# Optimization experiments

Measured on AMD Instinct MI355X. Metric: run time of the kernel, lower is better.

## Reference

```python
import jax, jax.numpy as jnp
import numpy as np

BN_EPS = 1e-3  # keras BatchNormalization default epsilon


def conv1x1(x, w):
    # x: [N,C,H,W], w: [O,C] (1x1 conv, no bias)
    return jnp.einsum('nchw,oc->nohw', x, w)


def bn(x, gamma, beta, mean, var):
    # inference-mode batchnorm over channel axis 1
    scale = gamma / jnp.sqrt(var + BN_EPS)
    shift = beta - mean * scale
    return x * scale[None, :, None, None] + shift[None, :, None, None]


def fourier_unit(x, w, gamma, beta, mean, var):
    # x: [N,C,H,W] NCHW. 1D rfft over W (matches tf.signal.rfft), normalized by sqrt(W).
    N, C, H, W = x.shape
    norm = jnp.sqrt(jnp.float32(W))
    f = jnp.fft.rfft(x / norm, axis=-1)          # [N,C,H,Wf] complex64, Wf=W//2+1
    Wf = f.shape[-1]
    # interleave re/im per channel: [N,C,2,H,Wf] -> [N,2C,H,Wf]
    ff = jnp.stack([jnp.real(f), jnp.imag(f)], axis=2).reshape(N, 2 * C, H, Wf)
    y = jax.nn.relu(bn(conv1x1(ff, w), gamma, beta, mean, var))  # [N,2C,H,Wf]
    Co = y.shape[1] // 2
    y = y.reshape(N, Co, 2, H, Wf)
    c = jax.lax.complex(y[:, :, 0], y[:, :, 1])
    return jnp.fft.irfft(c, n=W, axis=-1) * norm  # [N,Co,H,W]


def setup_inputs() -> dict:
    key = jax.random.key(0)
    ks = jax.random.split(key, 20)
    N, H, W, Cin = 8, 128, 128, 256
    fmaps = 256
    half = fmaps // 2  # 128

    def nrm(k, shape, s=0.05):
        return jax.random.normal(k, shape, dtype=jnp.float32) * s

    def bn_params(k, c):
        k1, k2, k3, k4 = jax.random.split(k, 4)
        gamma = jax.random.uniform(k1, (c,), dtype=jnp.float32) + 0.5
        beta = nrm(k2, (c,), 0.1)
        mean = nrm(k3, (c,), 0.1)
        var = jax.random.uniform(k4, (c,), dtype=jnp.float32) + 0.5
        return gamma, beta, mean, var

    x = jax.random.normal(ks[0], (N, H, W, Cin), dtype=jnp.float32)
    w1 = nrm(ks[1], (half, Cin))
    g1, b1, m1, v1 = bn_params(ks[2], half)
    fu_w = nrm(ks[3], (2 * half, 2 * half))
    fu_g, fu_b, fu_m, fu_v = bn_params(ks[4], 2 * half)
    lfu_w = nrm(ks[5], (2 * half, 2 * half))
    lfu_g, lfu_b, lfu_m, lfu_v = bn_params(ks[6], 2 * half)
    w2 = nrm(ks[7], (fmaps, half))
    return {
        'x': x, 'w1': w1, 'g1': g1, 'b1': b1, 'm1': m1, 'v1': v1,
        'fu_w': fu_w, 'fu_g': fu_g, 'fu_b': fu_b, 'fu_m': fu_m, 'fu_v': fu_v,
        'lfu_w': lfu_w, 'lfu_g': lfu_g, 'lfu_b': lfu_b, 'lfu_m': lfu_m, 'lfu_v': lfu_v,
        'w2': w2,
    }


def reference(x, w1, g1, b1, m1, v1,
              fu_w, fu_g, fu_b, fu_m, fu_v,
              lfu_w, lfu_g, lfu_b, lfu_m, lfu_v,
              w2):
    # NHWC -> NCHW (stride=1, no downsample)
    x = jnp.transpose(x, (0, 3, 1, 2))
    x = jax.nn.relu(bn(conv1x1(x, w1), g1, b1, m1, v1))  # [N,half,H,W]
    out = fourier_unit(x, fu_w, fu_g, fu_b, fu_m, fu_v)
    # local fourier unit: take first C//4 channels, fold 2x2 spatial patches into channels
    C = x.shape[1]
    xs = x[:, :C // 4]
    xs = jnp.concatenate(jnp.split(xs, 2, axis=2), axis=1)  # split H
    xs = jnp.concatenate(jnp.split(xs, 2, axis=3), axis=1)  # split W -> [N,C,H/2,W/2]
    xs = fourier_unit(xs, lfu_w, lfu_g, lfu_b, lfu_m, lfu_v)
    xs = jnp.tile(xs, (1, 1, 2, 2))  # back to [N,C,H,W]
    out = conv1x1(x + out + xs, w2)  # [N,fmaps,H,W]
    return jnp.transpose(out, (0, 2, 3, 1))  # NCHW -> NHWC
```

## Files before the change

kernel.cpp:

```cpp
#include <hip/hip_runtime.h>
#include <math.h>

typedef __attribute__((ext_vector_type(8))) short short8;
typedef __attribute__((ext_vector_type(4))) float f32x4;
typedef __attribute__((ext_vector_type(16))) float f32x16;

#define SW7b(r) (((r) & 7) << 4)
#define SW3b(r) (((r) & 3) << 4)
#define K15(r) (((r) & 15) << 4)
#define K7(r)  (((r) & 7) << 4)

static __device__ __forceinline__ unsigned short f2b(float f){
  unsigned u = __float_as_uint(f);
  u = (u + 0x7FFFu + ((u >> 16) & 1u)) >> 16;
  return (unsigned short)u;
}
static __device__ __forceinline__ float b2f(unsigned short u){
  return __uint_as_float(((unsigned)u) << 16);
}
static __device__ __forceinline__ void gl16(const void* g, void* l) {
  __builtin_amdgcn_global_load_lds(
      (const __attribute__((address_space(1))) void*)g,
      (__attribute__((address_space(3))) void*)l, 16, 0, 0);
}

__global__ void k_wt(const float* __restrict__ w1, const float* __restrict__ fu_w,
                     const float* __restrict__ lfu_w, const float* __restrict__ w2,
                     const float* __restrict__ g1, const float* __restrict__ b1,
                     const float* __restrict__ m1, const float* __restrict__ v1,
                     const float* __restrict__ fg, const float* __restrict__ fb,
                     const float* __restrict__ fm, const float* __restrict__ fv,
                     const float* __restrict__ lg_, const float* __restrict__ lb_,
                     const float* __restrict__ lm_, const float* __restrict__ lv_,
                     unsigned short* __restrict__ w1b, unsigned short* __restrict__ fuwb,
                     unsigned short* __restrict__ lfuwb, unsigned short* __restrict__ w2b,
                     unsigned short* __restrict__ DFTf, unsigned short* __restrict__ IDFTf,
                     unsigned short* __restrict__ DFTl, unsigned short* __restrict__ IDFTl,
                     float* __restrict__ sc1, float* __restrict__ sh1,
                     float* __restrict__ scF, float* __restrict__ shF,
                     float* __restrict__ scL, float* __restrict__ shL) {
  int t = blockIdx.x * 256 + threadIdx.x;
  const float TPI = 6.283185307179586f;
  if (t < 32768) {
    { int co = t >> 8, k = t & 255; w1b[co * 256 + (k ^ ((co & 7) << 3))] = f2b(w1[t]); }
    { int co = t >> 7, k = t & 127; w2b[co * 128 + (k ^ ((co & 15) << 3))] = f2b(w2[t]); }
  }
  if (t < 65536) {
    int co = t >> 8, k = t & 255;
    fuwb[(size_t)(k >> 6) * 16384 + co * 64 + ((k & 63) ^ ((co & 7) << 3))] = f2b(fu_w[t]);
    lfuwb[co * 256 + (k ^ ((co & 7) << 3))] = f2b(lfu_w[t]);
  }
  if (t < 20480) {
    int m = t >> 7, w = t & 127; float v = 0.f;
    if (m < 130) {
      int wf = m >> 1; int ph = (wf * w) & 127;
      float ang = TPI * (float)ph / 128.f;
      v = ((m & 1) ? -sinf(ang) : cosf(ang)) * 0.08838834764831845f;
    }
    DFTf[m * 128 + (w ^ ((m & 15) << 3))] = f2b(v);
  }
  if (t < 24576) {
    int m = t / 192, k2 = t % 192; float v = 0.f;
    if (k2 < 130) {
      int wf = k2 >> 1; float a = (wf == 0 || wf == 64) ? 1.f : 2.f;
      int ph = (wf * m) & 127;
      float ang = TPI * (float)ph / 128.f;
      v = ((k2 & 1) ? -a * sinf(ang) : a * cosf(ang)) * 0.08838834764831845f;
    }
    IDFTf[m * 192 + (k2 ^ ((m & 7) << 3))] = f2b(v);
  }
  if (t < 5120) {
    int m = t >> 6, w = t & 63; float v = 0.f;
    if (m < 66) {
      int wf = m >> 1; int ph = (wf * w) & 63;
      float ang = TPI * (float)ph / 64.f;
      v = ((m & 1) ? -sinf(ang) : cosf(ang)) * 0.125f;
    }
    DFTl[m * 64 + (w ^ ((m & 7) << 3))] = f2b(v);
  }
  if (t < 6144) {
    int m = t / 96, k2 = t % 96; float v = 0.f;
    if (k2 < 66) {
      int wf = k2 >> 1; float a = (wf == 0 || wf == 32) ? 1.f : 2.f;
      int ph = (wf * m) & 63;
      float ang = TPI * (float)ph / 64.f;
      v = ((k2 & 1) ? -a * sinf(ang) : a * cosf(ang)) * 0.125f;
    }
    IDFTl[m * 96 + (k2 ^ ((m & 3) << 3))] = f2b(v);
  }
  if (t < 128) { float s = g1[t] * rsqrtf(v1[t] + 1e-3f); sc1[t] = s; sh1[t] = b1[t] - m1[t] * s; }
  if (t < 256) { float s = fg[t] * rsqrtf(fv[t] + 1e-3f); scF[t] = s; shF[t] = fb[t] - fm[t] * s; }
  if (t < 256) { float s = lg_[t] * rsqrtf(lv_[t] + 1e-3f); scL[t] = s; shL[t] = lb_[t] - lm_[t] * s; }
}

__global__ __launch_bounds__(512) void k_conv1(const unsigned short* __restrict__ A,
                                               const float* __restrict__ x,
                                               unsigned short* __restrict__ X1c,
                                               const float* __restrict__ scp,
                                               const float* __restrict__ shp) {
  __shared__ __align__(16) char A_s[128 * 512];
  __shared__ __align__(16) char B_s[2][32768];
  int t = threadIdx.x; int wid = t >> 6, l = t & 63;
  int wm = wid >> 2, wn = wid & 3;
  int m0 = wm * 64, n0 = wn * 64;
  int lr = l & 15, lg = l >> 4;
  size_t nh0 = (size_t)blockIdx.x * 2;
  const char* Ab = (const char*)A;
  const char* xrow = (const char*)(x + nh0 * 32768);
  #pragma unroll
  for (int i = 0; i < 8; i++) { int g = i * 512 + t; gl16(Ab + g * 16, A_s + g * 16); }
  #pragma unroll
  for (int i = 0; i < 4; i++) {
    int g = i * 512 + t; int w = g >> 3, o = g & 7;
    gl16(xrow + (size_t)w * 1024 + ((o * 16) ^ SW7b(w)), B_s[0] + g * 16);
  }
  f32x4 acc[4][4];
  #pragma unroll
  for (int mt = 0; mt < 4; mt++)
    #pragma unroll
    for (int nt = 0; nt < 4; nt++) acc[mt][nt] = (f32x4){0.f, 0.f, 0.f, 0.f};
  __syncthreads();
  for (int it = 0; it < 8; it++) {
    int kk = it * 32;
    if (it < 7) {
      #pragma unroll
      for (int i = 0; i < 4; i++) {
        int g = i * 512 + t; int w = g >> 3, o = g & 7;
        gl16(xrow + (size_t)w * 1024 + (kk + 32) * 4 + ((o * 16) ^ SW7b(w)),
             B_s[(it + 1) & 1] + g * 16);
      }
    }
    const char* Bc = B_s[it & 1];
    short8 af[4], bf[4];
    #pragma unroll
    for (int mt = 0; mt < 4; mt++) {
      int m = m0 + 16 * mt + lr;
      af[mt] = *(const short8*)(A_s + m * 512 + ((kk * 2 + lg * 16) ^ SW7b(m)));
    }
    #pragma unroll
    for (int nt = 0; nt < 4; nt++) {
      int w = n0 + 16 * nt + lr;
      float4 f0 = *(const float4*)(Bc + w * 128 + ((lg * 32) ^ SW7b(w)));
      float4 f1 = *(const float4*)(Bc + w * 128 + ((lg * 32 + 16) ^ SW7b(w)));
      short8 bb;
      bb[0] = (short)f2b(f0.x); bb[1] = (short)f2b(f0.y);
      bb[2] = (short)f2b(f0.z); bb[3] = (short)f2b(f0.w);
      bb[4] = (short)f2b(f1.x); bb[5] = (short)f2b(f1.y);
      bb[6] = (short)f2b(f1.z); bb[7] = (short)f2b(f1.w);
      bf[nt] = bb;
    }
    #pragma unroll
    for (int mt = 0; mt < 4; mt++)
      #pragma unroll
      for (int nt = 0; nt < 4; nt++)
        acc[mt][nt] = __builtin_amdgcn_mfma_f32_16x16x32_bf16(af[mt], bf[nt], acc[mt][nt], 0, 0, 0);
    __syncthreads();
  }
  #pragma unroll
  for (int nt = 0; nt < 4; nt++) {
    int wcol = n0 + 16 * nt + lr;
    char* xout = (char*)X1c + (nh0 + (wcol >> 7)) * 32768;
    int w = wcol & 127;
    #pragma unroll
    for (int mt = 0; mt < 4; mt++) {
      int rb = m0 + 16 * mt + lg * 4;
      float4 s4 = *(const float4*)&scp[rb];
      float4 h4 = *(const float4*)&shp[rb];
      f32x4 v = acc[mt][nt];
      *(unsigned short*)(xout + (rb + 0) * 256 + ((w * 2) ^ K15(rb + 0))) = f2b(fmaxf(v[0] * s4.x + h4.x, 0.f));
      *(unsigned short*)(xout + (rb + 1) * 256 + ((w * 2) ^ K15(rb + 1))) = f2b(fmaxf(v[1] * s4.y + h4.y, 0.f));
      *(unsigned short*)(xout + (rb + 2) * 256 + ((w * 2) ^ K15(rb + 2))) = f2b(fmaxf(v[2] * s4.z + h4.z, 0.f));
      *(unsigned short*)(xout + (rb + 3) * 256 + ((w * 2) ^ K15(rb + 3))) = f2b(fmaxf(v[3] * s4.w + h4.w, 0.f));
    }
  }
}

__global__ __launch_bounds__(256) void k_lfu(const unsigned short* __restrict__ DFTm,
                                             const unsigned short* __restrict__ lfuw,
                                             const unsigned short* __restrict__ IDFTm,
                                             const unsigned short* __restrict__ X1c,
                                             const float* __restrict__ scp,
                                             const float* __restrict__ shp,
                                             unsigned short* __restrict__ XSO) {
  __shared__ __align__(16) char SH[81920];
  char* M   = SH;
  char* Xs  = SH + 16384;
  char* FFl = SH + 32768;
  char* Yl  = SH + 57344;
  int t = threadIdx.x, wid = t >> 6, l = t & 63, lr = l & 15, lg = l >> 4;
  int b = blockIdx.x; int n = b >> 6, h2 = b & 63;
  {
    const char* src = (const char*)DFTm;
    #pragma unroll
    for (int i = 0; i < 3; i++) { int g = i * 256 + t; if (g < 640) gl16(src + g * 16, M + g * 16); }
    #pragma unroll
    for (int i = 0; i < 4; i++) {
      int g = i * 256 + t; int c2 = g >> 3, o = g & 7;
      int c0 = c2 & 31, hb = (c2 >> 5) & 1, wbq = (c2 >> 6) & 1;
      int half = wbq ^ ((c0 >> 3) & 1);
      const char* s = (const char*)X1c +
          ((size_t)(n * 128 + hb * 64 + h2) * 128 + c0) * 256 + half * 128 + o * 16;
      gl16(s, Xs + g * 16);
    }
    #pragma unroll
    for (int i = 0; i < 8; i++) {
      int u = i * 256 + t;
      if (u < 1920) *(unsigned*)(FFl + 33 * 512 + u * 4) = 0u;
    }
  }
  __syncthreads();
  {
    f32x4 acc[5][2];
    #pragma unroll
    for (int mt = 0; mt < 5; mt++) { acc[mt][0] = (f32x4){0,0,0,0}; acc[mt][1] = (f32x4){0,0,0,0}; }
    for (int kk = 0; kk < 64; kk += 32) {
      int kb = kk * 2 + lg * 16;
      short8 bf[2];
      #pragma unroll
      for (int nt = 0; nt < 2; nt++) {
        int c2 = wid * 32 + 16 * nt + lr;
        bf[nt] = *(const short8*)(Xs + c2 * 128 + (kb ^ SW7b(c2)));
      }
      #pragma unroll
      for (int mt = 0; mt < 5; mt++) {
        int m = 16 * mt + lr;
        short8 af = *(const short8*)(M + m * 128 + (kb ^ SW7b(m)));
        #pragma unroll
        for (int nt = 0; nt < 2; nt++)
          acc[mt][nt] = __builtin_amdgcn_mfma_f32_16x16x32_bf16(af, bf[nt], acc[mt][nt], 0, 0, 0);
      }
    }
    #pragma unroll
    for (int nt = 0; nt < 2; nt++) {
      int c2 = wid * 32 + 16 * nt + lr;
      #pragma unroll
      for (int mt = 0; mt < 5; mt++) {
        int rb = 16 * mt + lg * 4;
        int wf0 = rb >> 1;
        f32x4 v = acc[mt][nt];
        if (wf0 < 33) {
          unsigned pk = (unsigned)f2b(v[0]) | ((unsigned)f2b(v[1]) << 16);
          *(unsigned*)(FFl + wf0 * 512 + ((4 * c2) ^ SW7b(wf0))) = pk;
        }
        if (wf0 + 1 < 33) {
          unsigned pk = (unsigned)f2b(v[2]) | ((unsigned)f2b(v[3]) << 16);
          *(unsigned*)(FFl + (wf0 + 1) * 512 + ((4 * c2) ^ SW7b(wf0 + 1))) = pk;
        }
      }
    }
  }
  __syncthreads();
  int wm2 = wid >> 1, wn2 = wid & 1;
  for (int ch = 0; ch < 8; ch++) {
    {
      const char* src = (const char*)lfuw + (size_t)ch * 16384;
      #pragma unroll
      for (int i = 0; i < 4; i++) { int g = i * 256 + t; gl16(src + g * 16, M + g * 16); }
    }
    __syncthreads();
    int NT = wn2 ? 1 : 2;
    f32x4 acc[2];
    acc[0] = (f32x4){0,0,0,0}; acc[1] = (f32x4){0,0,0,0};
    int lm = wm2 * 16 + lr;
    for (int kk = 0; kk < 256; kk += 32) {
      int kb = kk * 2 + lg * 16;
      short8 af = *(const short8*)(M + lm * 512 + (kb ^ SW7b(lm)));
      #pragma unroll
      for (int j = 0; j < 2; j++) {
        if (j < NT) {
          int wf = wn2 * 32 + 16 * j + lr;
          short8 bf = *(const short8*)(FFl + wf * 512 + (kb ^ SW7b(wf)));
          acc[j] = __builtin_amdgcn_mfma_f32_16x16x32_bf16(af, bf, acc[j], 0, 0, 0);
        }
      }
    }
    int co = ch * 32 + wm2 * 16 + lg * 4;
    float4 s4 = *(const float4*)&scp[co];
    float4 h4 = *(const float4*)&shp[co];
    int cc0 = co >> 1;
    #pragma unroll
    for (int j = 0; j < 2; j++) {
      if (j < NT) {
        int wf = wn2 * 32 + 16 * j + lr;
        f32x4 v = acc[j];
        float v0 = fmaxf(v[0] * s4.x + h4.x, 0.f);
        float v1 = fmaxf(v[1] * s4.y + h4.y, 0.f);
        float v2 = fmaxf(v[2] * s4.z + h4.z, 0.f);
        float v3 = fmaxf(v[3] * s4.w + h4.w, 0.f);
        unsigned p0 = (unsigned)f2b(v0) | ((unsigned)f2b(v1) << 16);
        unsigned p1 = (unsigned)f2b(v2) | ((unsigned)f2b(v3) << 16);
        *(unsigned*)(Yl + (cc0 + 0) * 192 + ((4 * wf) ^ SW3b(cc0 + 0))) = p0;
        *(unsigned*)(Yl + (cc0 + 1) * 192 + ((4 * wf) ^ SW3b(cc0 + 1))) = p1;
      }
    }
    __syncthreads();
  }
  {
    const char* src = (const char*)IDFTm;
    #pragma unroll
    for (int i = 0; i < 3; i++) { int g = i * 256 + t; gl16(src + g * 16, M + g * 16); }
  }
  __syncthreads();
  {
    f32x4 acc[8];
    #pragma unroll
    for (int nt = 0; nt < 8; nt++) acc[nt] = (f32x4){0,0,0,0};
    int w = wid * 16 + lr;
    for (int kk = 0; kk < 96; kk += 32) {
      int kb = kk * 2 + lg * 16;
      short8 af = *(const short8*)(M + w * 192 + (kb ^ SW3b(w)));
      #pragma unroll
      for (int nt = 0; nt < 8; nt++) {
        int cc = 16 * nt + lr;
        short8 bf = *(const short8*)(Yl + cc * 192 + (kb ^ SW3b(cc)));
        acc[nt] = __builtin_amdgcn_mfma_f32_16x16x32_bf16(af, bf, acc[nt], 0, 0, 0);
      }
    }
    int w0 = wid * 16 + lg * 4;
    #pragma unroll
    for (int nt = 0; nt < 8; nt++) {
      int cc = 16 * nt + lr;
      f32x4 v = acc[nt];
      ushort4 o;
      o.x = f2b(v[0]); o.y = f2b(v[1]); o.z = f2b(v[2]); o.w = f2b(v[3]);
      *(ushort4*)(XSO + (((size_t)n * 128 + cc) * 64 + h2) * 64 + w0) = o;
    }
  }
}

__global__ __launch_bounds__(1024, 4) void k_fu(const unsigned short* __restrict__ DFTm,
                                                const unsigned short* __restrict__ fuw,
                                                const unsigned short* __restrict__ IDFTm,
                                                const unsigned short* __restrict__ w2m,
                                                const unsigned short* __restrict__ X1c,
                                                const unsigned short* __restrict__ XSO,
                                                const float* __restrict__ scF,
                                                const float* __restrict__ shF,
                                                float* __restrict__ out) {
  __shared__ __align__(16) char SH[161792];
  char* R0 = SH;
  char* R1 = SH + 40960;
  char* R2 = SH + 73728;
  char* R3 = SH + 122880;
  int t = threadIdx.x, wid = t >> 6, l = t & 63;
  int lc = l & 31, hf = l >> 5;
  size_t nh = blockIdx.x;
  int n = (int)(nh >> 7), hh = (int)(nh & 127);
  const char* xb = (const char*)X1c + nh * 32768;

  #pragma unroll
  for (int i = 0; i < 3; i++) {
    int g = i * 1024 + t;
    if (g < 2560) gl16((const char*)DFTm + (size_t)g * 16, R0 + g * 16);
  }
  *(unsigned*)(R2 + 80 * 512 + t * 8) = 0u;
  *(unsigned*)(R2 + 80 * 512 + t * 8 + 4) = 0u;
  __syncthreads();
  {
    #pragma unroll
    for (int i = 0; i < 2; i++) {
      int g = i * 1024 + t;
      gl16((const char*)fuw + (size_t)g * 16, R1 + g * 16);
    }
    int mb = wid & 3, nb = wid >> 2;
    int c = nb * 32 + lc;
    short8 bfp[8];
    #pragma unroll
    for (int ks = 0; ks < 8; ks++)
      bfp[ks] = *(const short8*)(xb + (size_t)c * 256 + ((ks * 32 + hf * 16) ^ K15(c)));
    f32x16 acc0 = {0}, acc1 = {0};
    bool x2 = (wid < 4);
    int c2b = wid * 32 + lc;
    #pragma unroll
    for (int ks = 0; ks < 8; ks++) {
      int ko = ks * 32 + hf * 16;
      int m = mb * 32 + lc;
      short8 af = *(const short8*)(R0 + (size_t)m * 256 + (ko ^ K15(m)));
      acc0 = __builtin_amdgcn_mfma_f32_32x32x16_bf16(af, bfp[ks], acc0, 0, 0, 0);
      if (x2) {
        int m2 = 128 + lc;
        short8 af2 = *(const short8*)(R0 + (size_t)m2 * 256 + (ko ^ K15(m2)));
        short8 bf2 = *(const short8*)(xb + (size_t)c2b * 256 + (ko ^ K15(c2b)));
        acc1 = __builtin_amdgcn_mfma_f32_32x32x16_bf16(af2, bf2, acc1, 0, 0, 0);
      }
    }
    #pragma unroll
    for (int q = 0; q < 4; q++) {
      int wfe = mb * 16 + 4 * q + 2 * hf;
      unsigned p0 = (unsigned)f2b(acc0[4 * q + 0]) | ((unsigned)f2b(acc0[4 * q + 1]) << 16);
      unsigned p1 = (unsigned)f2b(acc0[4 * q + 2]) | ((unsigned)f2b(acc0[4 * q + 3]) << 16);
      *(unsigned*)(R2 + (size_t)wfe * 512 + ((4 * c) ^ K15(wfe))) = p0;
      *(unsigned*)(R2 + (size_t)(wfe + 1) * 512 + ((4 * c) ^ K15(wfe + 1))) = p1;
    }
    if (x2) {
      #pragma unroll
      for (int q = 0; q < 4; q++) {
        int wfe = 64 + 4 * q + 2 * hf;
        unsigned p0 = (unsigned)f2b(acc1[4 * q + 0]) | ((unsigned)f2b(acc1[4 * q + 1]) << 16);
        unsigned p1 = (unsigned)f2b(acc1[4 * q + 2]) | ((unsigned)f2b(acc1[4 * q + 3]) << 16);
        *(unsigned*)(R2 + (size_t)wfe * 512 + ((4 * c2b) ^ K15(wfe))) = p0;
        *(unsigned*)(R2 + (size_t)(wfe + 1) * 512 + ((4 * c2b) ^ K15(wfe + 1))) = p1;
      }
    }
  }
  {
    int mb = wid >> 1, odd = wid & 1;
    int co = mb * 32 + lc;
    f32x16 pa = {0}, pb = {0};
    int wfA = (odd ? 32 : 0) + lc;
    int wfB = 64 + lc;
    #pragma unroll
    for (int ch = 0; ch < 4; ch++) {
      char* Mc = (ch & 1) ? R0 : R1;
      char* Mn = (ch & 1) ? R1 : R0;
      __syncthreads();
      if (ch < 3) {
        #pragma unroll
        for (int i = 0; i < 2; i++) {
          int g = i * 1024 + t;
          gl16((const char*)fuw + (size_t)(ch + 1) * 32768 + (size_t)g * 16, Mn + g * 16);
        }
      } else {
        #pragma unroll
        for (int i = 0; i < 2; i++) {
          int g = i * 1024 + t;
          gl16((const char*)w2m + (size_t)g * 16, Mn + g * 16);
        }
      }
      #pragma unroll
      for (int ks = 0; ks < 4; ks++) {
        int ko = ks * 32 + hf * 16;
        short8 af = *(const short8*)(Mc + (size_t)co * 128 + (ko ^ K7(co)));
        int kg = (ch * 4 + ks) * 32 + hf * 16;
        short8 bfA = *(const short8*)(R2 + (size_t)wfA * 512 + (kg ^ K15(wfA)));
        pa = __builtin_amdgcn_mfma_f32_32x32x16_bf16(af, bfA, pa, 0, 0, 0);
        if (!odd) {
          short8 bfB = *(const short8*)(R2 + (size_t)wfB * 512 + (kg ^ K15(wfB)));
          pb = __builtin_amdgcn_mfma_f32_32x32x16_bf16(af, bfB, pb, 0, 0, 0);
        }
      }
    }
    #pragma unroll
    for (int q = 0; q < 4; q++) {
      int co0 = mb * 32 + 8 * q + 4 * hf;
      float4 s4 = *(const float4*)&scF[co0];
      float4 h4 = *(const float4*)&shF[co0];
      int cc0 = co0 >> 1;
      {
        float v0 = fmaxf(pa[4 * q + 0] * s4.x + h4.x, 0.f);
        float v1 = fmaxf(pa[4 * q + 1] * s4.y + h4.y, 0.f);
        float v2 = fmaxf(pa[4 * q + 2] * s4.z + h4.z, 0.f);
        float v3 = fmaxf(pa[4 * q + 3] * s4.w + h4.w, 0.f);
        unsigned p0 = (unsigned)f2b(v0) | ((unsigned)f2b(v1) << 16);
        unsigned p1 = (unsigned)f2b(v2) | ((unsigned)f2b(v3) << 16);
        *(unsigned*)(R3 + (size_t)(cc0 + 0) * 304 + 4 * wfA) = p0;
        *(unsigned*)(R3 + (size_t)(cc0 + 1) * 304 + 4 * wfA) = p1;
      }
      if (!odd && lc < 12) {
        float v0 = fmaxf(pb[4 * q + 0] * s4.x + h4.x, 0.f);
        float v1 = fmaxf(pb[4 * q + 1] * s4.y + h4.y, 0.f);
        float v2 = fmaxf(pb[4 * q + 2] * s4.z + h4.z, 0.f);
        float v3 = fmaxf(pb[4 * q + 3] * s4.w + h4.w, 0.f);
        unsigned p0 = (unsigned)f2b(v0) | ((unsigned)f2b(v1) << 16);
        unsigned p1 = (unsigned)f2b(v2) | ((unsigned)f2b(v3) << 16);
        *(unsigned*)(R3 + (size_t)(cc0 + 0) * 304 + 4 * wfB) = p0;
        *(unsigned*)(R3 + (size_t)(cc0 + 1) * 304 + 4 * wfB) = p1;
      }
    }
  }
  __syncthreads();
  #pragma unroll
  for (int i = 0; i < 3; i++) {
    int g = i * 1024 + t;
    gl16((const char*)IDFTm + (size_t)g * 16, R2 + g * 16);
  }
  #pragma unroll
  for (int i = 0; i < 2; i++) {
    int g = i * 1024 + t;
    gl16((const char*)w2m + 32768 + (size_t)g * 16, R0 + g * 16);
  }
  __syncthreads();
  {
    int mb = wid & 3, nb = wid >> 2;
    int mw = mb * 32 + lc;
    int cc = nb * 32 + lc;
    f32x16 p3 = {0};
    #pragma unroll
    for (int ks = 0; ks < 9; ks++) {
      int ko = ks * 32 + hf * 16;
      short8 af = *(const short8*)(R2 + (size_t)mw * 384 + (ko ^ K7(mw)));
      short8 bf = *(const short8*)(R3 + (size_t)cc * 304 + ko);
      p3 = __builtin_amdgcn_mfma_f32_32x32x16_bf16(af, bf, p3, 0, 0, 0);
    }
    ushort4 rx[4], rs[4];
    #pragma unroll
    for (int q = 0; q < 4; q++) {
      int w0 = mb * 32 + 8 * q + 4 * hf;
      rx[q] = *(const ushort4*)(xb + (size_t)cc * 256 + ((2 * w0) ^ K15(cc)));
      rs[q] = *(const ushort4*)(XSO + (((size_t)n * 128 + cc) * 64 + (hh & 63)) * 64 + (w0 & 63));
    }
    __syncthreads();
    #pragma unroll
    for (int q = 0; q < 4; q++) {
      int w0 = mb * 32 + 8 * q + 4 * hf;
      float f0 = p3[4 * q + 0] + b2f(rx[q].x) + b2f(rs[q].x);
      float f1 = p3[4 * q + 1] + b2f(rx[q].y) + b2f(rs[q].y);
      float f2_ = p3[4 * q + 2] + b2f(rx[q].z) + b2f(rs[q].z);
      float f3 = p3[4 * q + 3] + b2f(rx[q].w) + b2f(rs[q].w);
      *(unsigned short*)(R3 + (size_t)(w0 + 0) * 256 + ((2 * cc) ^ K15(w0 + 0))) = f2b(f0);
      *(unsigned short*)(R3 + (size_t)(w0 + 1) * 256 + ((2 * cc) ^ K15(w0 + 1))) = f2b(f1);
      *(unsigned short*)(R3 + (size_t)(w0 + 2) * 256 + ((2 * cc) ^ K15(w0 + 2))) = f2b(f2_);
      *(unsigned short*)(R3 + (size_t)(w0 + 3) * 256 + ((2 * cc) ^ K15(w0 + 3))) = f2b(f3);
    }
  }
  __syncthreads();
  {
    int mb = wid & 3, nb = wid >> 2;
    int mco = mb * 32 + lc;
    int nw = nb * 32 + lc;
    #pragma unroll
    for (int ck = 0; ck < 2; ck++) {
      const char* Mc = ck ? R0 : R1;
      f32x16 p4 = {0};
      #pragma unroll
      for (int ks = 0; ks < 8; ks++) {
        int ko = ks * 32 + hf * 16;
        short8 af = *(const short8*)(Mc + (size_t)mco * 256 + (ko ^ K15(mco)));
        short8 bf = *(const short8*)(R3 + (size_t)nw * 256 + (ko ^ K15(nw)));
        p4 = __builtin_amdgcn_mfma_f32_32x32x16_bf16(af, bf, p4, 0, 0, 0);
      }
      #pragma unroll
      for (int q = 0; q < 4; q++) {
        int co2 = ck * 128 + mb * 32 + 8 * q + 4 * hf;
        float4 o;
        o.x = p4[4 * q + 0]; o.y = p4[4 * q + 1];
        o.z = p4[4 * q + 2]; o.w = p4[4 * q + 3];
        *(float4*)(out + (nh * 128 + nw) * 256 + co2) = o;
      }
    }
  }
}

extern "C" void kernel_launch(void* const* d_in, const int* in_sizes, int n_in,
                              void* d_out, int out_size, void* d_ws, size_t ws_size,
                              hipStream_t stream) {
  const float* x     = (const float*)d_in[0];
  const float* w1    = (const float*)d_in[1];
  const float* g1    = (const float*)d_in[2];
  const float* b1    = (const float*)d_in[3];
  const float* m1    = (const float*)d_in[4];
  const float* v1    = (const float*)d_in[5];
  const float* fu_w  = (const float*)d_in[6];
  const float* fu_g  = (const float*)d_in[7];
  const float* fu_b  = (const float*)d_in[8];
  const float* fu_m  = (const float*)d_in[9];
  const float* fu_v  = (const float*)d_in[10];
  const float* lfu_w = (const float*)d_in[11];
  const float* lfu_g = (const float*)d_in[12];
  const float* lfu_b = (const float*)d_in[13];
  const float* lfu_m = (const float*)d_in[14];
  const float* lfu_v = (const float*)d_in[15];
  const float* w2    = (const float*)d_in[16];
  float* out = (float*)d_out;

  char* p = (char*)d_ws;
  unsigned short* X1c = (unsigned short*)p; p += 33554432;
  unsigned short* XSO = (unsigned short*)p; p += 8388608;
  unsigned short* w1b   = (unsigned short*)p; p += 65536;
  unsigned short* fuwb  = (unsigned short*)p; p += 131072;
  unsigned short* lfuwb = (unsigned short*)p; p += 131072;
  unsigned short* w2b   = (unsigned short*)p; p += 65536;
  unsigned short* DFTf  = (unsigned short*)p; p += 40960;
  unsigned short* IDFTf = (unsigned short*)p; p += 49152;
  unsigned short* DFTl  = (unsigned short*)p; p += 10240;
  unsigned short* IDFTl = (unsigned short*)p; p += 12288;
  float* sc1 = (float*)p; p += 512;
  float* sh1 = (float*)p; p += 512;
  float* scF = (float*)p; p += 1024;
  float* shF = (float*)p; p += 1024;
  float* scL = (float*)p; p += 1024;
  float* shL = (float*)p; p += 1024;

  k_wt<<<dim3(256), dim3(256), 0, stream>>>(w1, fu_w, lfu_w, w2, g1, b1, m1, v1,
                                            fu_g, fu_b, fu_m, fu_v, lfu_g, lfu_b, lfu_m, lfu_v,
                                            w1b, fuwb, lfuwb, w2b, DFTf, IDFTf, DFTl, IDFTl,
                                            sc1, sh1, scF, shF, scL, shL);
  k_conv1<<<dim3(512), dim3(512), 0, stream>>>(w1b, x, X1c, sc1, sh1);
  k_lfu<<<dim3(512), dim3(256), 0, stream>>>(DFTl, lfuwb, IDFTl, X1c, scL, shL, XSO);
  k_fu<<<dim3(1024), dim3(1024), 0, stream>>>(DFTf, fuwb, IDFTf, w2b, X1c, XSO, scF, shF, out);
}
```

Baseline: 148.0 us.

## Double-buffer LFU weight chunks and prefetch IDFT matrix in k_lfu

The per-chunk LFU weight loads are double-buffered between two LDS regions: the next chunk, or the IDFT matrix on the last iteration, is issued before the current chunk's MFMA loop. This removes one barrier and one exposed load per iteration, plus the separate IDFT load stage. The forward-DFT B operand is now read straight from global memory into registers instead of being staged through LDS, which frees that region for the second weight buffer. The trade-off is that the X1c reads become uncoalesced per-lane global loads. Overlap also depends on the end-of-loop barrier waiting for the async LDS loads to finish.

```diff
diff --git a/kernel.cpp b/kernel.cpp
--- a/kernel.cpp
+++ b/kernel.cpp
@@ -184,24 +184,16 @@
                                              unsigned short* __restrict__ XSO) {
   __shared__ __align__(16) char SH[81920];
   char* M   = SH;
-  char* Xs  = SH + 16384;
+  char* S0  = SH + 16384;
   char* FFl = SH + 32768;
   char* Yl  = SH + 57344;
   int t = threadIdx.x, wid = t >> 6, l = t & 63, lr = l & 15, lg = l >> 4;
   int b = blockIdx.x; int n = b >> 6, h2 = b & 63;
   {
-    const char* src = (const char*)DFTm;
-    #pragma unroll
-    for (int i = 0; i < 3; i++) { int g = i * 256 + t; if (g < 640) gl16(src + g * 16, M + g * 16); }
-    #pragma unroll
-    for (int i = 0; i < 4; i++) {
-      int g = i * 256 + t; int c2 = g >> 3, o = g & 7;
-      int c0 = c2 & 31, hb = (c2 >> 5) & 1, wbq = (c2 >> 6) & 1;
-      int half = wbq ^ ((c0 >> 3) & 1);
-      const char* s = (const char*)X1c +
-          ((size_t)(n * 128 + hb * 64 + h2) * 128 + c0) * 256 + half * 128 + o * 16;
-      gl16(s, Xs + g * 16);
-    }
+    #pragma unroll
+    for (int i = 0; i < 3; i++) { int g = i * 256 + t; if (g < 640) gl16((const char*)DFTm + g * 16, M + g * 16); }
+    #pragma unroll
+    for (int i = 0; i < 4; i++) { int g = i * 256 + t; gl16((const char*)lfuw + g * 16, S0 + g * 16); }
     #pragma unroll
     for (int i = 0; i < 8; i++) {
       int u = i * 256 + t;
@@ -210,24 +202,33 @@
   }
   __syncthreads();
   {
+    short8 bfp[2][2];
+    #pragma unroll
+    for (int nt = 0; nt < 2; nt++) {
+      int c2 = wid * 32 + 16 * nt + lr;
+      int c0 = c2 & 31, hb = (c2 >> 5) & 1, wbq = (c2 >> 6) & 1;
+      int half = wbq ^ ((c0 >> 3) & 1);
+      const char* base = (const char*)X1c +
+          ((size_t)(n * 128 + hb * 64 + h2) * 128 + c0) * 256 + half * 128;
+      #pragma unroll
+      for (int ki = 0; ki < 2; ki++) {
+        int kb = ki * 64 + lg * 16;
+        bfp[nt][ki] = *(const short8*)(base + (kb ^ SW7b(c2)));
+      }
+    }
     f32x4 acc[5][2];
     #pragma unroll
     for (int mt = 0; mt < 5; mt++) { acc[mt][0] = (f32x4){0,0,0,0}; acc[mt][1] = (f32x4){0,0,0,0}; }
-    for (int kk = 0; kk < 64; kk += 32) {
-      int kb = kk * 2 + lg * 16;
-      short8 bf[2];
-      #pragma unroll
-      for (int nt = 0; nt < 2; nt++) {
-        int c2 = wid * 32 + 16 * nt + lr;
-        bf[nt] = *(const short8*)(Xs + c2 * 128 + (kb ^ SW7b(c2)));
-      }
+    #pragma unroll
+    for (int ki = 0; ki < 2; ki++) {
+      int kb = ki * 64 + lg * 16;
       #pragma unroll
       for (int mt = 0; mt < 5; mt++) {
         int m = 16 * mt + lr;
         short8 af = *(const short8*)(M + m * 128 + (kb ^ SW7b(m)));
         #pragma unroll
         for (int nt = 0; nt < 2; nt++)
-          acc[mt][nt] = __builtin_amdgcn_mfma_f32_16x16x32_bf16(af, bf[nt], acc[mt][nt], 0, 0, 0);
+          acc[mt][nt] = __builtin_amdgcn_mfma_f32_16x16x32_bf16(af, bfp[nt][ki], acc[mt][nt], 0, 0, 0);
       }
     }
     #pragma unroll
@@ -252,19 +253,28 @@
   __syncthreads();
   int wm2 = wid >> 1, wn2 = wid & 1;
   for (int ch = 0; ch < 8; ch++) {
-    {
-      const char* src = (const char*)lfuw + (size_t)ch * 16384;
-      #pragma unroll
-      for (int i = 0; i < 4; i++) { int g = i * 256 + t; gl16(src + g * 16, M + g * 16); }
-    }
-    __syncthreads();
+    char* Mc = (ch & 1) ? M : S0;
+    char* Mn = (ch & 1) ? S0 : M;
+    if (ch < 7) {
+      #pragma unroll
+      for (int i = 0; i < 4; i++) {
+        int g = i * 256 + t;
+        gl16((const char*)lfuw + (size_t)(ch + 1) * 16384 + g * 16, Mn + g * 16);
+      }
+    } else {
+      #pragma unroll
+      for (int i = 0; i < 3; i++) {
+        int g = i * 256 + t;
+        if (g < 768) gl16((const char*)IDFTm + g * 16, Mn + g * 16);
+      }
+    }
     int NT = wn2 ? 1 : 2;
     f32x4 acc[2];
     acc[0] = (f32x4){0,0,0,0}; acc[1] = (f32x4){0,0,0,0};
     int lm = wm2 * 16 + lr;
     for (int kk = 0; kk < 256; kk += 32) {
       int kb = kk * 2 + lg * 16;
-      short8 af = *(const short8*)(M + lm * 512 + (kb ^ SW7b(lm)));
+      short8 af = *(const short8*)(Mc + lm * 512 + (kb ^ SW7b(lm)));
       #pragma unroll
       for (int j = 0; j < 2; j++) {
         if (j < NT) {
@@ -296,19 +306,13 @@
     __syncthreads();
   }
   {
-    const char* src = (const char*)IDFTm;
-    #pragma unroll
-    for (int i = 0; i < 3; i++) { int g = i * 256 + t; gl16(src + g * 16, M + g * 16); }
-  }
-  __syncthreads();
-  {
     f32x4 acc[8];
     #pragma unroll
     for (int nt = 0; nt < 8; nt++) acc[nt] = (f32x4){0,0,0,0};
     int w = wid * 16 + lr;
     for (int kk = 0; kk < 96; kk += 32) {
       int kb = kk * 2 + lg * 16;
-      short8 af = *(const short8*)(M + w * 192 + (kb ^ SW3b(w)));
+      short8 af = *(const short8*)(S0 + w * 192 + (kb ^ SW3b(w)));
       #pragma unroll
       for (int nt = 0; nt < 8; nt++) {
         int cc = 16 * nt + lr;
```

Result: no change. 145.7 us (-1.6%).
